# Optimization experiments

Hardware: AMD Instinct MI355X
Metric: run time of the kernel (lower is better)

## Reference

```python
import jax, jax.numpy as jnp
import numpy as np

BN_EPS = 1e-5

def _conv(x, W, b, stride, pad):
    # x: [B,C,H,W], W: [O,I,kh,kw]
    y = jax.lax.conv_general_dilated(
        x, W, window_strides=(stride, stride),
        padding=[(pad, pad), (pad, pad)],
        dimension_numbers=('NCHW', 'OIHW', 'NCHW'))
    return y + b[None, :, None, None]

def _bn(x, gamma, beta, mean, var):
    inv = gamma * jax.lax.rsqrt(var + BN_EPS)
    return x * inv[None, :, None, None] + (beta - mean * inv)[None, :, None, None]

def _haar_cD(x):
    # pywt.dwt2(x, 'haar') diagonal detail over last two axes (even H,W):
    # cD[i,j] = (x[2i,2j] - x[2i,2j+1] - x[2i+1,2j] + x[2i+1,2j+1]) / 2
    a = x[..., 0::2, 0::2]
    b = x[..., 0::2, 1::2]
    c = x[..., 1::2, 0::2]
    d = x[..., 1::2, 1::2]
    return (a - b - c + d) * 0.5

def setup_inputs() -> dict:
    key = jax.random.key(0)
    ks = jax.random.split(key, 20)
    B = 8192
    f32 = jnp.float32
    inp = {
        'x':   jax.random.normal(ks[0], (B, 3, 32, 32), dtype=f32),
        # conv1: 3 -> 32, k5 s2 p2
        'w1':  jax.random.normal(ks[1], (32, 3, 5, 5), dtype=f32) * 0.05,
        'b1':  jnp.zeros((32,), f32),
        'g1':  jnp.ones((32,), f32),
        'be1': jnp.zeros((32,), f32),
        'm1':  jax.random.normal(ks[2], (32,), dtype=f32) * 0.1,
        'v1':  jax.random.uniform(ks[3], (32,), dtype=f32, minval=0.5, maxval=1.5),
        # conv2: 32 -> 64, k3 s2 p1
        'w2':  jax.random.normal(ks[4], (64, 32, 3, 3), dtype=f32) * 0.05,
        'b2':  jnp.zeros((64,), f32),
        'g2':  jnp.ones((64,), f32),
        'be2': jnp.zeros((64,), f32),
        'm2':  jax.random.normal(ks[5], (64,), dtype=f32) * 0.1,
        'v2':  jax.random.uniform(ks[6], (64,), dtype=f32, minval=0.5, maxval=1.5),
        # attention conv: 64 -> 1, k1
        'wa':  jax.random.normal(ks[7], (1, 64, 1, 1), dtype=f32) * 0.1,
        'ba':  jnp.zeros((1,), f32),
        # decoder linears (torch Linear layout: [out, in])
        'wd1': jax.random.normal(ks[8], (512, 64 * 8 * 8), dtype=f32) * 0.02,
        'bd1': jnp.zeros((512,), f32),
        'wd2': jax.random.normal(ks[9], (128, 512), dtype=f32) * 0.04,
        'bd2': jnp.zeros((128,), f32),
    }
    return inp

def reference(x, w1, b1, g1, be1, m1, v1, w2, b2, g2, be2, m2, v2,
              wa, ba, wd1, bd1, wd2, bd2):
    # wavelet_conv stem
    h = jax.nn.relu(_bn(_conv(x, w1, b1, 2, 2), g1, be1, m1, v1))   # [B,32,16,16]
    feat = jax.nn.relu(_bn(_conv(h, w2, b2, 2, 1), g2, be2, m2, v2))  # [B,64,8,8]
    # Haar DWT diagonal-detail gate (detached in the original)
    cD = jax.lax.stop_gradient(_haar_cD(feat))                        # [B,64,4,4]
    cD_up = jnp.repeat(jnp.repeat(cD, 2, axis=-2), 2, axis=-1)        # [B,64,8,8]
    feat = feat * cD_up
    # attention gate
    attn = jax.nn.sigmoid(_conv(feat, wa, ba, 1, 0))                  # [B,1,8,8]
    feat = feat * attn
    # decode
    f = feat.reshape(feat.shape[0], -1)                               # [B,4096]
    h1 = jax.nn.relu(f @ wd1.T + bd1)                                  # [B,512]
    return jax.nn.sigmoid(h1 @ wd2.T + bd2)                            # [B,128]
```

## Files before the change

### kernel.cpp

```cpp
#include <hip/hip_runtime.h>
#include <hip/hip_bf16.h>

typedef __bf16 bf16x8 __attribute__((ext_vector_type(8)));
typedef float f32x4 __attribute__((ext_vector_type(4)));

#define BN_EPS 1e-5f

__device__ __forceinline__ void gl_lds16(const __bf16* g, __bf16* l) {
    __builtin_amdgcn_global_load_lds(
        (const __attribute__((address_space(1))) unsigned int*)g,
        (__attribute__((address_space(3))) unsigned int*)l,
        16, 0, 0);
}

__global__ void cvt_kernel(const float* __restrict__ a, __bf16* __restrict__ o, int n) {
    int i = blockIdx.x * blockDim.x + threadIdx.x;
    int stride = gridDim.x * blockDim.x;
    for (; i < n; i += stride) o[i] = (__bf16)a[i];
}

__global__ void w1r_kernel(const float* __restrict__ w1, __bf16* __restrict__ o) {
    int i = blockIdx.x * 256 + threadIdx.x;
    if (i < 4096) {
        int oc = i >> 7, rem = i & 127;
        int ot = rem >> 3, j = rem & 7;
        float v = 0.f;
        if (ot < 15 && j < 5) {
            int ic = ot / 5, ky = ot % 5;
            v = w1[((oc * 3 + ic) * 5 + ky) * 5 + j];
        }
        o[i] = (__bf16)v;
    }
}

__global__ void w2r_kernel(const float* __restrict__ w2, __bf16* __restrict__ o) {
    int i = blockIdx.x * 256 + threadIdx.x;
    if (i < 64 * 288) {
        int oc = i / 288, rem = i % 288;
        int tap = rem / 32, ic = rem % 32;
        o[i] = (__bf16)w2[(oc * 32 + ic) * 9 + tap];
    }
}

__global__ __launch_bounds__(256, 4) void conv_fused_kernel(
    const float* __restrict__ x,
    const __bf16* __restrict__ w1r, const float* __restrict__ b1,
    const float* __restrict__ g1, const float* __restrict__ be1,
    const float* __restrict__ m1, const float* __restrict__ v1,
    const __bf16* __restrict__ w2r, const float* __restrict__ b2,
    const float* __restrict__ g2, const float* __restrict__ be2,
    const float* __restrict__ m2, const float* __restrict__ v2,
    const float* __restrict__ wa, const float* __restrict__ ba,
    __bf16* __restrict__ f)
{
    union UA { float xs[3][36][40]; float feat[64][64]; };
    struct PB { float cd[64][16]; float attn[4][64]; };
    union UB { __bf16 hs[289 * 40]; PB pb; };
    __shared__ __align__(16) UA ua;
    __shared__ __align__(16) UB ub;

    const int b    = blockIdx.x;
    const int tid  = threadIdx.x;
    const int lane = tid & 63;
    const int wave = tid >> 6;
    const int lo   = lane >> 4;
    const int ln   = lane & 15;

    float* xsf = &ua.xs[0][0][0];
    __bf16* hsf = ub.hs;

    {
        float4* xp = (float4*)xsf;
        for (int i = tid; i < 1080; i += 256) xp[i] = float4{0.f, 0.f, 0.f, 0.f};
        if (tid < 132) {
            int pi = tid >> 2, ch = tid & 3;
            int pix = (pi < 17) ? pi : (pi - 16) * 17;
            bf16x8 z = {};
            *(bf16x8*)&hsf[pix * 40 + ch * 8] = z;
        }
    }
    __syncthreads();

    {
        const float4* xb = (const float4*)(x + (size_t)b * 3072);
        #pragma unroll
        for (int r = 0; r < 3; ++r) {
            int c = r * 256 + tid;
            int plane = c >> 8, rem = c & 255;
            int row = rem >> 3, c4 = rem & 7;
            *(float4*)&ua.xs[plane][row + 2][4 + c4 * 4] = xb[c];
        }
    }

    bf16x8 bw1[2][4];
    #pragma unroll
    for (int nt = 0; nt < 2; ++nt)
        #pragma unroll
        for (int s = 0; s < 4; ++s)
            bw1[nt][s] = *(const bf16x8*)(w1r + (nt * 16 + ln) * 128 + (s * 4 + lo) * 8);
    __syncthreads();

    f32x4 c1[4][2] = {};
    #pragma unroll
    for (int s = 0; s < 4; ++s) {
        const int o  = s * 4 + lo;
        const int ic = (o * 205) >> 10;
        const int ky = o - ic * 5;
        const bool dummy = (o == 15);
        const int icc = dummy ? 2 : ic;
        const int cbase = icc * 1440 + 2 * ln + 2;
        #pragma unroll
        for (int mt = 0; mt < 4; ++mt) {
            const int oy  = wave * 4 + mt;
            const int row = dummy ? 35 : (2 * oy + ky);
            const int idx = cbase + row * 40;
            float2 p0 = *(const float2*)&xsf[idx];
            float2 p1 = *(const float2*)&xsf[idx + 2];
            float  p2 = xsf[idx + 4];
            bf16x8 af;
            af[0] = (__bf16)p0.x; af[1] = (__bf16)p0.y;
            af[2] = (__bf16)p1.x; af[3] = (__bf16)p1.y;
            af[4] = (__bf16)p2;
            af[5] = (__bf16)0.f; af[6] = (__bf16)0.f; af[7] = (__bf16)0.f;
            #pragma unroll
            for (int nt = 0; nt < 2; ++nt)
                c1[mt][nt] = __builtin_amdgcn_mfma_f32_16x16x32_bf16(af, bw1[nt][s], c1[mt][nt], 0, 0, 0);
        }
    }

    #pragma unroll
    for (int nt = 0; nt < 2; ++nt) {
        const int oc  = nt * 16 + ln;
        const float inv = g1[oc] * rsqrtf(v1[oc] + BN_EPS);
        const float bb  = be1[oc] + (b1[oc] - m1[oc]) * inv;
        #pragma unroll
        for (int mt = 0; mt < 4; ++mt) {
            const int hy = wave * 4 + mt + 1;
            #pragma unroll
            for (int r = 0; r < 4; ++r) {
                const int hx = lo * 4 + r + 1;
                hsf[(hy * 17 + hx) * 40 + oc] = (__bf16)fmaxf(c1[mt][nt][r] * inv + bb, 0.f);
            }
        }
    }

    const int wm = wave >> 1, wn = wave & 1;
    bf16x8 bw2[2][9];
    #pragma unroll
    for (int nt = 0; nt < 2; ++nt) {
        const __bf16* wp = w2r + (wn * 32 + nt * 16 + ln) * 288 + lo * 8;
        #pragma unroll
        for (int ks = 0; ks < 9; ++ks)
            bw2[nt][ks] = *(const bf16x8*)(wp + ks * 32);
    }
    __syncthreads();

    f32x4 c2[2][2] = {};
    {
        int pixbase[2];
        #pragma unroll
        for (int mt = 0; mt < 2; ++mt) {
            int p = wm * 32 + mt * 16 + ln;
            int qy = p >> 3, qx = p & 7;
            pixbase[mt] = (2 * qy * 17 + 2 * qx) * 40 + lo * 8;
        }
        #pragma unroll
        for (int ks = 0; ks < 9; ++ks) {
            const int ty = ks / 3, tx = ks % 3;
            bf16x8 af[2];
            #pragma unroll
            for (int mt = 0; mt < 2; ++mt)
                af[mt] = *(const bf16x8*)&hsf[pixbase[mt] + (ty * 17 + tx) * 40];
            #pragma unroll
            for (int mt = 0; mt < 2; ++mt)
                #pragma unroll
                for (int nt = 0; nt < 2; ++nt)
                    c2[mt][nt] = __builtin_amdgcn_mfma_f32_16x16x32_bf16(af[mt], bw2[nt][ks], c2[mt][nt], 0, 0, 0);
        }
    }

    #pragma unroll
    for (int nt = 0; nt < 2; ++nt) {
        const int oc  = wn * 32 + nt * 16 + ln;
        const float inv = g2[oc] * rsqrtf(v2[oc] + BN_EPS);
        const float bb  = be2[oc] + (b2[oc] - m2[oc]) * inv;
        #pragma unroll
        for (int mt = 0; mt < 2; ++mt)
            #pragma unroll
            for (int r = 0; r < 4; ++r) {
                const int p = wm * 32 + mt * 16 + lo * 4 + r;
                ua.feat[oc][p] = fmaxf(c2[mt][nt][r] * inv + bb, 0.f);
            }
    }
    __syncthreads();

    #pragma unroll
    for (int r = 0; r < 4; ++r) {
        int idx = tid * 4 + r;
        int c = idx >> 4, yx = idx & 15;
        int y = yx >> 2, xx = yx & 3;
        float aa = ua.feat[c][(2 * y) * 8 + 2 * xx];
        float bb = ua.feat[c][(2 * y) * 8 + 2 * xx + 1];
        float cc = ua.feat[c][(2 * y + 1) * 8 + 2 * xx];
        float dd = ua.feat[c][(2 * y + 1) * 8 + 2 * xx + 1];
        ub.pb.cd[c][yx] = 0.5f * (aa - bb - cc + dd);
    }
    __syncthreads();

    const int q  = tid & 63;
    const int g  = wave;
    const int qy = q >> 3, qx = q & 7;
    const int qq = (qy >> 1) * 4 + (qx >> 1);
    float a2[16];
    float part = 0.f;
    #pragma unroll
    for (int j = 0; j < 16; ++j) {
        int oc = g * 16 + j;
        float v = ua.feat[oc][q] * ub.pb.cd[oc][qq];
        a2[j] = v;
        part += v * wa[oc];
    }
    ub.pb.attn[g][q] = part;
    __syncthreads();
    float s2  = ub.pb.attn[0][q] + ub.pb.attn[1][q] + ub.pb.attn[2][q] + ub.pb.attn[3][q] + ba[0];
    float sig = 1.f / (1.f + __expf(-s2));

    __bf16* fb = f + (size_t)b * 4096;
    #pragma unroll
    for (int j = 0; j < 16; ++j)
        fb[(g * 16 + j) * 64 + q] = (__bf16)(a2[j] * sig);
}

__global__ __launch_bounds__(256) void gemm1_kernel(
    const __bf16* __restrict__ A, const __bf16* __restrict__ B,
    const float* __restrict__ bias, __bf16* __restrict__ C)
{
    const int K = 4096, NOUT = 512;
    __shared__ __align__(16) __bf16 As[128][64];
    __shared__ __align__(16) __bf16 Bs[64][64];
    const int tid  = threadIdx.x;
    const int lane = tid & 63;
    const int wave = tid >> 6;
    const int wm = wave >> 1, wn = wave & 1;
    const int lo = lane >> 4, ln = lane & 15;
    const int m0 = blockIdx.x * 128, n0 = blockIdx.y * 64;
    const int sw = ln & 7;
    f32x4 acc[4][2] = {};
    for (int k0 = 0; k0 < K; k0 += 64) {
        #pragma unroll
        for (int r = 0; r < 4; ++r) {
            int i = r * 256 + tid;
            int row = i >> 3, cs = i & 7;
            gl_lds16(A + (size_t)(m0 + row) * K + k0 + (cs ^ (row & 7)) * 8,
                     &As[0][0] + i * 8);
        }
        #pragma unroll
        for (int r = 0; r < 2; ++r) {
            int i = r * 256 + tid;
            int row = i >> 3, cs = i & 7;
            gl_lds16(B + (size_t)(n0 + row) * K + k0 + (cs ^ (row & 7)) * 8,
                     &Bs[0][0] + i * 8);
        }
        __syncthreads();
        #pragma unroll
        for (int s = 0; s < 2; ++s) {
            const int c = s * 4 + lo;
            const int slot = (c ^ sw) * 8;
            bf16x8 af[4], bfr[2];
            #pragma unroll
            for (int mt = 0; mt < 4; ++mt)
                af[mt] = *(const bf16x8*)(&As[wm * 64 + mt * 16 + ln][slot]);
            #pragma unroll
            for (int nt = 0; nt < 2; ++nt)
                bfr[nt] = *(const bf16x8*)(&Bs[wn * 32 + nt * 16 + ln][slot]);
            #pragma unroll
            for (int mt = 0; mt < 4; ++mt)
                #pragma unroll
                for (int nt = 0; nt < 2; ++nt)
                    acc[mt][nt] = __builtin_amdgcn_mfma_f32_16x16x32_bf16(af[mt], bfr[nt], acc[mt][nt], 0, 0, 0);
        }
        __syncthreads();
    }
    #pragma unroll
    for (int mt = 0; mt < 4; ++mt)
        #pragma unroll
        for (int nt = 0; nt < 2; ++nt)
            #pragma unroll
            for (int r = 0; r < 4; ++r) {
                int m = m0 + wm * 64 + mt * 16 + lo * 4 + r;
                int n = n0 + wn * 32 + nt * 16 + ln;
                float v = acc[mt][nt][r] + bias[n];
                C[(size_t)m * NOUT + n] = (__bf16)fmaxf(v, 0.f);
            }
}

__global__ __launch_bounds__(256) void gemm2_kernel(
    const __bf16* __restrict__ A, const __bf16* __restrict__ B,
    const float* __restrict__ bias, float* __restrict__ Out)
{
    const int K = 512, NOUT = 128;
    __shared__ __align__(16) __bf16 As[64][64];
    __shared__ __align__(16) __bf16 Bs[128][64];
    const int tid  = threadIdx.x;
    const int lane = tid & 63;
    const int wave = tid >> 6;
    const int lo = lane >> 4, ln = lane & 15;
    const int m0 = blockIdx.x * 64;
    const int sw = ln & 7;
    f32x4 acc[4][2] = {};
    for (int k0 = 0; k0 < K; k0 += 64) {
        #pragma unroll
        for (int r = 0; r < 2; ++r) {
            int i = r * 256 + tid;
            int row = i >> 3, cs = i & 7;
            gl_lds16(A + (size_t)(m0 + row) * K + k0 + (cs ^ (row & 7)) * 8,
                     &As[0][0] + i * 8);
        }
        #pragma unroll
        for (int r = 0; r < 4; ++r) {
            int i = r * 256 + tid;
            int row = i >> 3, cs = i & 7;
            gl_lds16(B + (size_t)row * K + k0 + (cs ^ (row & 7)) * 8,
                     &Bs[0][0] + i * 8);
        }
        __syncthreads();
        #pragma unroll
        for (int s = 0; s < 2; ++s) {
            const int c = s * 4 + lo;
            const int slot = (c ^ sw) * 8;
            bf16x8 af[4], bfr[2];
            #pragma unroll
            for (int mt = 0; mt < 4; ++mt)
                af[mt] = *(const bf16x8*)(&As[mt * 16 + ln][slot]);
            #pragma unroll
            for (int nt = 0; nt < 2; ++nt)
                bfr[nt] = *(const bf16x8*)(&Bs[wave * 32 + nt * 16 + ln][slot]);
            #pragma unroll
            for (int mt = 0; mt < 4; ++mt)
                #pragma unroll
                for (int nt = 0; nt < 2; ++nt)
                    acc[mt][nt] = __builtin_amdgcn_mfma_f32_16x16x32_bf16(af[mt], bfr[nt], acc[mt][nt], 0, 0, 0);
        }
        __syncthreads();
    }
    #pragma unroll
    for (int mt = 0; mt < 4; ++mt)
        #pragma unroll
        for (int nt = 0; nt < 2; ++nt)
            #pragma unroll
            for (int r = 0; r < 4; ++r) {
                int m = m0 + mt * 16 + lo * 4 + r;
                int n = wave * 32 + nt * 16 + ln;
                float v = acc[mt][nt][r] + bias[n];
                Out[(size_t)m * NOUT + n] = 1.f / (1.f + __expf(-v));
            }
}

extern "C" void kernel_launch(void* const* d_in, const int* in_sizes, int n_in,
                              void* d_out, int out_size, void* d_ws, size_t ws_size,
                              hipStream_t stream)
{
    const float* x   = (const float*)d_in[0];
    const float* w1  = (const float*)d_in[1];
    const float* b1  = (const float*)d_in[2];
    const float* g1  = (const float*)d_in[3];
    const float* be1 = (const float*)d_in[4];
    const float* m1  = (const float*)d_in[5];
    const float* v1  = (const float*)d_in[6];
    const float* w2  = (const float*)d_in[7];
    const float* b2  = (const float*)d_in[8];
    const float* g2  = (const float*)d_in[9];
    const float* be2 = (const float*)d_in[10];
    const float* m2  = (const float*)d_in[11];
    const float* v2  = (const float*)d_in[12];
    const float* wa  = (const float*)d_in[13];
    const float* ba  = (const float*)d_in[14];
    const float* wd1 = (const float*)d_in[15];
    const float* bd1 = (const float*)d_in[16];
    const float* wd2 = (const float*)d_in[17];
    const float* bd2 = (const float*)d_in[18];

    char* ws = (char*)d_ws;
    __bf16* f_bf   = (__bf16*)(ws);
    __bf16* h1_bf  = (__bf16*)(ws + 67108864);
    __bf16* wd1_bf = (__bf16*)(ws + 67108864 + 8388608);
    __bf16* wd2_bf = (__bf16*)(ws + 67108864 + 8388608 + 4194304);
    __bf16* w2r_bf = (__bf16*)(ws + 67108864 + 8388608 + 4194304 + 131072);
    __bf16* w1r_bf = (__bf16*)(ws + 67108864 + 8388608 + 4194304 + 131072 + 65536);

    cvt_kernel<<<2048, 256, 0, stream>>>(wd1, wd1_bf, 512 * 4096);
    cvt_kernel<<<64, 256, 0, stream>>>(wd2, wd2_bf, 128 * 512);
    w1r_kernel<<<16, 256, 0, stream>>>(w1, w1r_bf);
    w2r_kernel<<<72, 256, 0, stream>>>(w2, w2r_bf);

    conv_fused_kernel<<<8192, 256, 0, stream>>>(x, w1r_bf, b1, g1, be1, m1, v1,
                                                w2r_bf, b2, g2, be2, m2, v2, wa, ba, f_bf);

    dim3 g3(64, 8);
    gemm1_kernel<<<g3, 256, 0, stream>>>(f_bf, wd1_bf, bd1, h1_bf);

    gemm2_kernel<<<128, 256, 0, stream>>>(h1_bf, wd2_bf, bd2, (float*)d_out);
}
```

Before: 317.2 us.

## Shrink conv LDS with bf16 input staging, vectorize feature stores, retile GEMM1

The input tile is staged in LDS as bf16 instead of fp32, and the conv buffers are merged into one smaller buffer so five blocks can fit per CU (launch bounds raised from 4 to 5). The flattened feature output is now written in position-major order with 16-byte vector stores. To match, wd1 is permuted by a new transpose kernel during weight prep. The small weight-prep kernels are merged into one launch, and GEMM1 switches to 64x128 tiles. Risks are bf16 rounding of the input in LDS, which matches the conversion done before, and an extra barrier added before the feat writes.

```diff
diff --git a/kernel.cpp b/kernel.cpp
--- a/kernel.cpp
+++ b/kernel.cpp
@@ -2,6 +2,7 @@
 #include <hip/hip_bf16.h>
 
 typedef __bf16 bf16x8 __attribute__((ext_vector_type(8)));
+typedef __bf16 bf16x4 __attribute__((ext_vector_type(4)));
 typedef float f32x4 __attribute__((ext_vector_type(4)));
 
 #define BN_EPS 1e-5f
@@ -13,14 +14,32 @@
         16, 0, 0);
 }
 
-__global__ void cvt_kernel(const float* __restrict__ a, __bf16* __restrict__ o, int n) {
-    int i = blockIdx.x * blockDim.x + threadIdx.x;
-    int stride = gridDim.x * blockDim.x;
-    for (; i < n; i += stride) o[i] = (__bf16)a[i];
-}
-
-__global__ void w1r_kernel(const float* __restrict__ w1, __bf16* __restrict__ o) {
+__global__ __launch_bounds__(256) void wd1p_kernel(const float* __restrict__ wd1, __bf16* __restrict__ o) {
+    __shared__ float t2[64][65];
+    const int n = blockIdx.x;
+    const int tid = threadIdx.x;
+    const float* src = wd1 + (size_t)n * 4096;
+    #pragma unroll
+    for (int r = 0; r < 16; ++r) {
+        int j = r * 256 + tid;
+        t2[j & 63][j >> 6] = src[j];
+    }
+    __syncthreads();
+    __bf16* dst = o + (size_t)n * 4096;
+    #pragma unroll
+    for (int r = 0; r < 16; ++r) {
+        int t = r * 256 + tid;
+        dst[t] = (__bf16)t2[t >> 6][t & 63];
+    }
+}
+
+__global__ void prep_kernel(const float* __restrict__ wd2, const float* __restrict__ w1,
+                            const float* __restrict__ w2,
+                            __bf16* __restrict__ wd2o, __bf16* __restrict__ w1o,
+                            __bf16* __restrict__ w2o) {
     int i = blockIdx.x * 256 + threadIdx.x;
+    if (i < 65536) { wd2o[i] = (__bf16)wd2[i]; return; }
+    i -= 65536;
     if (i < 4096) {
         int oc = i >> 7, rem = i & 127;
         int ot = rem >> 3, j = rem & 7;
@@ -29,20 +48,18 @@
             int ic = ot / 5, ky = ot % 5;
             v = w1[((oc * 3 + ic) * 5 + ky) * 5 + j];
         }
-        o[i] = (__bf16)v;
-    }
-}
-
-__global__ void w2r_kernel(const float* __restrict__ w2, __bf16* __restrict__ o) {
-    int i = blockIdx.x * 256 + threadIdx.x;
-    if (i < 64 * 288) {
+        w1o[i] = (__bf16)v;
+        return;
+    }
+    i -= 4096;
+    if (i < 18432) {
         int oc = i / 288, rem = i % 288;
         int tap = rem / 32, ic = rem % 32;
-        o[i] = (__bf16)w2[(oc * 32 + ic) * 9 + tap];
-    }
-}
-
-__global__ __launch_bounds__(256, 4) void conv_fused_kernel(
+        w2o[i] = (__bf16)w2[(oc * 32 + ic) * 9 + tap];
+    }
+}
+
+__global__ __launch_bounds__(256, 5) void conv_fused_kernel(
     const float* __restrict__ x,
     const __bf16* __restrict__ w1r, const float* __restrict__ b1,
     const float* __restrict__ g1, const float* __restrict__ be1,
@@ -53,11 +70,12 @@
     const float* __restrict__ wa, const float* __restrict__ ba,
     __bf16* __restrict__ f)
 {
-    union UA { float xs[3][36][40]; float feat[64][64]; };
-    struct PB { float cd[64][16]; float attn[4][64]; };
-    union UB { __bf16 hs[289 * 40]; PB pb; };
-    __shared__ __align__(16) UA ua;
-    __shared__ __align__(16) UB ub;
+    __shared__ __align__(16) __bf16 xsb[3 * 36 * 40];
+    __shared__ __align__(16) char  ubuf[23120];
+    __bf16* hsf  = (__bf16*)ubuf;
+    float*  feat = (float*)ubuf;
+    float*  cds  = (float*)(ubuf + 16384);
+    float*  atn  = (float*)(ubuf + 20480);
 
     const int b    = blockIdx.x;
     const int tid  = threadIdx.x;
@@ -66,16 +84,12 @@
     const int lo   = lane >> 4;
     const int ln   = lane & 15;
 
-    float* xsf = &ua.xs[0][0][0];
-    __bf16* hsf = ub.hs;
-
     {
-        float4* xp = (float4*)xsf;
-        for (int i = tid; i < 1080; i += 256) xp[i] = float4{0.f, 0.f, 0.f, 0.f};
+        bf16x8 z = {};
+        for (int i = tid; i < 540; i += 256) *(bf16x8*)&xsb[i * 8] = z;
         if (tid < 132) {
             int pi = tid >> 2, ch = tid & 3;
             int pix = (pi < 17) ? pi : (pi - 16) * 17;
-            bf16x8 z = {};
             *(bf16x8*)&hsf[pix * 40 + ch * 8] = z;
         }
     }
@@ -88,7 +102,10 @@
             int c = r * 256 + tid;
             int plane = c >> 8, rem = c & 255;
             int row = rem >> 3, c4 = rem & 7;
-            *(float4*)&ua.xs[plane][row + 2][4 + c4 * 4] = xb[c];
+            float4 v = xb[c];
+            bf16x4 h;
+            h[0] = (__bf16)v.x; h[1] = (__bf16)v.y; h[2] = (__bf16)v.z; h[3] = (__bf16)v.w;
+            *(bf16x4*)&xsb[plane * 1440 + (row + 2) * 40 + 4 + c4 * 4] = h;
         }
     }
 
@@ -101,6 +118,7 @@
     __syncthreads();
 
     f32x4 c1[4][2] = {};
+    const unsigned int* xw = (const unsigned int*)xsb;
     #pragma unroll
     for (int s = 0; s < 4; ++s) {
         const int o  = s * 4 + lo;
@@ -108,23 +126,16 @@
         const int ky = o - ic * 5;
         const bool dummy = (o == 15);
         const int icc = dummy ? 2 : ic;
-        const int cbase = icc * 1440 + 2 * ln + 2;
         #pragma unroll
         for (int mt = 0; mt < 4; ++mt) {
             const int oy  = wave * 4 + mt;
             const int row = dummy ? 35 : (2 * oy + ky);
-            const int idx = cbase + row * 40;
-            float2 p0 = *(const float2*)&xsf[idx];
-            float2 p1 = *(const float2*)&xsf[idx + 2];
-            float  p2 = xsf[idx + 4];
-            bf16x8 af;
-            af[0] = (__bf16)p0.x; af[1] = (__bf16)p0.y;
-            af[2] = (__bf16)p1.x; af[3] = (__bf16)p1.y;
-            af[4] = (__bf16)p2;
-            af[5] = (__bf16)0.f; af[6] = (__bf16)0.f; af[7] = (__bf16)0.f;
+            const int dw  = icc * 720 + row * 20 + ln + 1;
+            union { unsigned int u[4]; bf16x8 v; } fa;
+            fa.u[0] = xw[dw]; fa.u[1] = xw[dw + 1]; fa.u[2] = xw[dw + 2]; fa.u[3] = 0;
             #pragma unroll
             for (int nt = 0; nt < 2; ++nt)
-                c1[mt][nt] = __builtin_amdgcn_mfma_f32_16x16x32_bf16(af, bw1[nt][s], c1[mt][nt], 0, 0, 0);
+                c1[mt][nt] = __builtin_amdgcn_mfma_f32_16x16x32_bf16(fa.v, bw1[nt][s], c1[mt][nt], 0, 0, 0);
         }
     }
 
@@ -178,6 +189,7 @@
                     c2[mt][nt] = __builtin_amdgcn_mfma_f32_16x16x32_bf16(af[mt], bw2[nt][ks], c2[mt][nt], 0, 0, 0);
         }
     }
+    __syncthreads();
 
     #pragma unroll
     for (int nt = 0; nt < 2; ++nt) {
@@ -189,7 +201,7 @@
             #pragma unroll
             for (int r = 0; r < 4; ++r) {
                 const int p = wm * 32 + mt * 16 + lo * 4 + r;
-                ua.feat[oc][p] = fmaxf(c2[mt][nt][r] * inv + bb, 0.f);
+                feat[oc * 64 + p] = fmaxf(c2[mt][nt][r] * inv + bb, 0.f);
             }
     }
     __syncthreads();
@@ -199,36 +211,41 @@
         int idx = tid * 4 + r;
         int c = idx >> 4, yx = idx & 15;
         int y = yx >> 2, xx = yx & 3;
-        float aa = ua.feat[c][(2 * y) * 8 + 2 * xx];
-        float bb = ua.feat[c][(2 * y) * 8 + 2 * xx + 1];
-        float cc = ua.feat[c][(2 * y + 1) * 8 + 2 * xx];
-        float dd = ua.feat[c][(2 * y + 1) * 8 + 2 * xx + 1];
-        ub.pb.cd[c][yx] = 0.5f * (aa - bb - cc + dd);
+        float aa = feat[c * 64 + (2 * y) * 8 + 2 * xx];
+        float bb = feat[c * 64 + (2 * y) * 8 + 2 * xx + 1];
+        float cc = feat[c * 64 + (2 * y + 1) * 8 + 2 * xx];
+        float dd = feat[c * 64 + (2 * y + 1) * 8 + 2 * xx + 1];
+        cds[c * 16 + yx] = 0.5f * (aa - bb - cc + dd);
     }
     __syncthreads();
 
     const int q  = tid & 63;
     const int g  = wave;
-    const int qy = q >> 3, qx = q & 7;
-    const int qq = (qy >> 1) * 4 + (qx >> 1);
+    const int qy2 = q >> 3, qx2 = q & 7;
+    const int qq = (qy2 >> 1) * 4 + (qx2 >> 1);
     float a2[16];
     float part = 0.f;
     #pragma unroll
     for (int j = 0; j < 16; ++j) {
         int oc = g * 16 + j;
-        float v = ua.feat[oc][q] * ub.pb.cd[oc][qq];
+        float v = feat[oc * 64 + q] * cds[oc * 16 + qq];
         a2[j] = v;
         part += v * wa[oc];
     }
-    ub.pb.attn[g][q] = part;
-    __syncthreads();
-    float s2  = ub.pb.attn[0][q] + ub.pb.attn[1][q] + ub.pb.attn[2][q] + ub.pb.attn[3][q] + ba[0];
+    atn[g * 64 + q] = part;
+    __syncthreads();
+    float s2  = atn[q] + atn[64 + q] + atn[128 + q] + atn[192 + q] + ba[0];
     float sig = 1.f / (1.f + __expf(-s2));
 
-    __bf16* fb = f + (size_t)b * 4096;
-    #pragma unroll
-    for (int j = 0; j < 16; ++j)
-        fb[(g * 16 + j) * 64 + q] = (__bf16)(a2[j] * sig);
+    bf16x8 fo0, fo1;
+    #pragma unroll
+    for (int j = 0; j < 8; ++j) {
+        fo0[j] = (__bf16)(a2[j] * sig);
+        fo1[j] = (__bf16)(a2[j + 8] * sig);
+    }
+    __bf16* fb = f + (size_t)b * 4096 + q * 64 + g * 16;
+    *(bf16x8*)fb = fo0;
+    *(bf16x8*)(fb + 8) = fo1;
 }
 
 __global__ __launch_bounds__(256) void gemm1_kernel(
@@ -236,30 +253,27 @@
     const float* __restrict__ bias, __bf16* __restrict__ C)
 {
     const int K = 4096, NOUT = 512;
-    __shared__ __align__(16) __bf16 As[128][64];
-    __shared__ __align__(16) __bf16 Bs[64][64];
+    __shared__ __align__(16) __bf16 As[64][64];
+    __shared__ __align__(16) __bf16 Bs[128][64];
     const int tid  = threadIdx.x;
     const int lane = tid & 63;
     const int wave = tid >> 6;
-    const int wm = wave >> 1, wn = wave & 1;
     const int lo = lane >> 4, ln = lane & 15;
-    const int m0 = blockIdx.x * 128, n0 = blockIdx.y * 64;
+    const int m0 = blockIdx.x * 64, n0 = blockIdx.y * 128;
     const int sw = ln & 7;
     f32x4 acc[4][2] = {};
     for (int k0 = 0; k0 < K; k0 += 64) {
         #pragma unroll
+        for (int r = 0; r < 2; ++r) {
+            int i = r * 256 + tid;
+            int row = i >> 3, cs = i & 7;
+            gl_lds16(A + (size_t)(m0 + row) * K + k0 + (cs ^ (row & 7)) * 8, &As[0][0] + i * 8);
+        }
+        #pragma unroll
         for (int r = 0; r < 4; ++r) {
             int i = r * 256 + tid;
             int row = i >> 3, cs = i & 7;
-            gl_lds16(A + (size_t)(m0 + row) * K + k0 + (cs ^ (row & 7)) * 8,
-                     &As[0][0] + i * 8);
-        }
-        #pragma unroll
-        for (int r = 0; r < 2; ++r) {
-            int i = r * 256 + tid;
-            int row = i >> 3, cs = i & 7;
-            gl_lds16(B + (size_t)(n0 + row) * K + k0 + (cs ^ (row & 7)) * 8,
-                     &Bs[0][0] + i * 8);
+            gl_lds16(B + (size_t)(n0 + row) * K + k0 + (cs ^ (row & 7)) * 8, &Bs[0][0] + i * 8);
         }
         __syncthreads();
         #pragma unroll
@@ -269,10 +283,10 @@
             bf16x8 af[4], bfr[2];
             #pragma unroll
             for (int mt = 0; mt < 4; ++mt)
-                af[mt] = *(const bf16x8*)(&As[wm * 64 + mt * 16 + ln][slot]);
+                af[mt] = *(const bf16x8*)(&As[mt * 16 + ln][slot]);
             #pragma unroll
             for (int nt = 0; nt < 2; ++nt)
-                bfr[nt] = *(const bf16x8*)(&Bs[wn * 32 + nt * 16 + ln][slot]);
+                bfr[nt] = *(const bf16x8*)(&Bs[wave * 32 + nt * 16 + ln][slot]);
             #pragma unroll
             for (int mt = 0; mt < 4; ++mt)
                 #pragma unroll
@@ -287,8 +301,8 @@
         for (int nt = 0; nt < 2; ++nt)
             #pragma unroll
             for (int r = 0; r < 4; ++r) {
-                int m = m0 + wm * 64 + mt * 16 + lo * 4 + r;
-                int n = n0 + wn * 32 + nt * 16 + ln;
+                int m = m0 + mt * 16 + lo * 4 + r;
+                int n = n0 + wave * 32 + nt * 16 + ln;
                 float v = acc[mt][nt][r] + bias[n];
                 C[(size_t)m * NOUT + n] = (__bf16)fmaxf(v, 0.f);
             }
@@ -313,15 +327,13 @@
         for (int r = 0; r < 2; ++r) {
             int i = r * 256 + tid;
             int row = i >> 3, cs = i & 7;
-            gl_lds16(A + (size_t)(m0 + row) * K + k0 + (cs ^ (row & 7)) * 8,
-                     &As[0][0] + i * 8);
+            gl_lds16(A + (size_t)(m0 + row) * K + k0 + (cs ^ (row & 7)) * 8, &As[0][0] + i * 8);
         }
         #pragma unroll
         for (int r = 0; r < 4; ++r) {
             int i = r * 256 + tid;
             int row = i >> 3, cs = i & 7;
-            gl_lds16(B + (size_t)row * K + k0 + (cs ^ (row & 7)) * 8,
-                     &Bs[0][0] + i * 8);
+            gl_lds16(B + (size_t)row * K + k0 + (cs ^ (row & 7)) * 8, &Bs[0][0] + i * 8);
         }
         __syncthreads();
         #pragma unroll
@@ -388,15 +400,13 @@
     __bf16* w2r_bf = (__bf16*)(ws + 67108864 + 8388608 + 4194304 + 131072);
     __bf16* w1r_bf = (__bf16*)(ws + 67108864 + 8388608 + 4194304 + 131072 + 65536);
 
-    cvt_kernel<<<2048, 256, 0, stream>>>(wd1, wd1_bf, 512 * 4096);
-    cvt_kernel<<<64, 256, 0, stream>>>(wd2, wd2_bf, 128 * 512);
-    w1r_kernel<<<16, 256, 0, stream>>>(w1, w1r_bf);
-    w2r_kernel<<<72, 256, 0, stream>>>(w2, w2r_bf);
+    prep_kernel<<<344, 256, 0, stream>>>(wd2, w1, w2, wd2_bf, w1r_bf, w2r_bf);
+    wd1p_kernel<<<512, 256, 0, stream>>>(wd1, wd1_bf);
 
     conv_fused_kernel<<<8192, 256, 0, stream>>>(x, w1r_bf, b1, g1, be1, m1, v1,
                                                 w2r_bf, b2, g2, be2, m2, v2, wa, ba, f_bf);
 
-    dim3 g3(64, 8);
+    dim3 g3(128, 4);
     gemm1_kernel<<<g3, 256, 0, stream>>>(f_bf, wd1_bf, bd1, h1_bf);
 
     gemm2_kernel<<<128, 256, 0, stream>>>(h1_bf, wd2_bf, bd2, (float*)d_out);
```

After: 314.9 us. No clear change (-0.7%).
